# Performance work log

Hardware: AMD Instinct MI355X
Metric: run time of the kernel (lower is better)

The kernel has to match this reference:

```python
import jax, jax.numpy as jnp
import numpy as np

NUM_CLASSES = 80
S = 7            # grid_size
NB = 2           # num_boxes per cell
LAMBDA_COORD = 5.0
LAMBDA_NOOBJ = 0.5
N_BOX = 20       # padded boxes per image


def setup_inputs() -> dict:
    key = jax.random.key(0)
    k1, k2, k3, k4 = jax.random.split(key, 4)
    B = 4096
    predictions = jax.random.uniform(k1, (B, S, S, NB, 5 + NUM_CLASSES), dtype=jnp.float32)
    # build valid normalized xyxy boxes: centers in [0.1,0.9], half-sizes in [0.01,0.085]
    centers = jax.random.uniform(k2, (B, N_BOX, 2), dtype=jnp.float32) * 0.8 + 0.1
    half = jax.random.uniform(k3, (B, N_BOX, 2), dtype=jnp.float32) * 0.075 + 0.01
    targets_boxes = jnp.concatenate([centers - half, centers + half], axis=-1)
    targets_labels = jax.random.randint(k4, (B, N_BOX), 0, NUM_CLASSES)
    return {"predictions": predictions, "targets_boxes": targets_boxes, "targets_labels": targets_labels}


def encode_targets(boxes, labels):
    # boxes: [B,N,4] xyxy normalized; labels: [B,N] int
    B, N, _ = boxes.shape
    x = (boxes[..., 0] + boxes[..., 2]) * 0.5
    y = (boxes[..., 1] + boxes[..., 3]) * 0.5
    w = boxes[..., 2] - boxes[..., 0]
    h = boxes[..., 3] - boxes[..., 1]
    j = jnp.clip(jnp.floor(x * S).astype(jnp.int32), 0, S - 1)
    i = jnp.clip(jnp.floor(y * S).astype(jnp.int32), 0, S - 1)
    x_cell = x * S - j
    y_cell = y * S - i
    onehot = jax.nn.one_hot(labels, NUM_CLASSES, dtype=boxes.dtype)
    feats = jnp.concatenate([x_cell[..., None], y_cell[..., None], w[..., None], h[..., None],
                             jnp.ones_like(x_cell)[..., None], onehot], axis=-1)  # [B,N,5+C]
    bidx = jnp.arange(B, dtype=jnp.int32)[:, None]
    flat = ((bidx * S + i) * S + j).ravel()                       # [B*N] cell ids
    order = jnp.broadcast_to(jnp.arange(N, dtype=jnp.int32), (B, N)).ravel()
    winner = jnp.full((B * S * S,), N, dtype=jnp.int32).at[flat].min(order)
    cell_b = jnp.arange(B * S * S, dtype=jnp.int32) // (S * S)
    sel = jnp.minimum(winner, N - 1)
    grid = feats[cell_b, sel]
    grid = jnp.where((winner < N)[:, None], grid, jnp.zeros_like(grid))
    return grid.reshape(B, S, S, 5 + NUM_CLASSES)


def iou_xywh(a, b):
    ax1 = a[..., 0] - a[..., 2] * 0.5; ay1 = a[..., 1] - a[..., 3] * 0.5
    ax2 = a[..., 0] + a[..., 2] * 0.5; ay2 = a[..., 1] + a[..., 3] * 0.5
    bx1 = b[..., 0] - b[..., 2] * 0.5; by1 = b[..., 1] - b[..., 3] * 0.5
    bx2 = b[..., 0] + b[..., 2] * 0.5; by2 = b[..., 1] + b[..., 3] * 0.5
    iw = jnp.clip(jnp.minimum(ax2, bx2) - jnp.maximum(ax1, bx1), 0.0)
    ih = jnp.clip(jnp.minimum(ay2, by2) - jnp.maximum(ay1, by1), 0.0)
    inter = iw * ih
    union = (ax2 - ax1) * (ay2 - ay1) + (bx2 - bx1) * (by2 - by1) - inter
    return inter / (union + 1e-6)


def yolo_loss(predictions, targets_boxes, targets_labels):
    B = predictions.shape[0]
    tg = encode_targets(targets_boxes, targets_labels)   # [B,S,S,5+C]
    txy, twh = tg[..., :2], tg[..., 2:4]
    tconf, tcls = tg[..., 4:5], tg[..., 5:]
    obj = (tconf[..., 0] > 0).astype(predictions.dtype)   # [B,S,S]
    # responsible box = argmax IoU per cell, masked by obj
    pred_boxes = predictions[..., 0:4]                     # [B,S,S,NB,4]
    tgt_boxes = jnp.concatenate([txy, twh], axis=-1)[:, :, :, None, :]
    ious = iou_xywh(pred_boxes, jnp.broadcast_to(tgt_boxes, pred_boxes.shape))  # [B,S,S,NB]
    best = jnp.argmax(ious, axis=-1)
    resp = jax.nn.one_hot(best, NB, dtype=predictions.dtype) * obj[..., None]   # [B,S,S,NB]
    pxy = predictions[..., 0:2]; pwh = predictions[..., 2:4]
    pconf = predictions[..., 4:5]; pcls = predictions[..., 5:]
    om = obj[..., None, None]        # [B,S,S,1,1]
    rm = resp[..., None]             # [B,S,S,NB,1]
    loss_xy = LAMBDA_COORD * jnp.sum(om * rm * (pxy - txy[:, :, :, None, :]) ** 2) / B
    loss_wh = LAMBDA_COORD * jnp.sum(om * rm * (jnp.sqrt(jnp.clip(pwh, 1e-6)) - jnp.sqrt(jnp.clip(twh[:, :, :, None, :], 1e-6))) ** 2) / B
    loss_conf_obj = jnp.sum(om * rm * (pconf - tconf[:, :, :, None, :]) ** 2) / B
    loss_conf_noobj = LAMBDA_NOOBJ * jnp.sum((1.0 - obj)[..., None, None] * pconf ** 2) / B
    pred_cls_resp = jnp.sum(pcls * rm, axis=3)             # [B,S,S,C]
    loss_cls = jnp.sum(obj[..., None] * (pred_cls_resp - tcls) ** 2) / B
    return loss_xy + loss_wh + loss_conf_obj + loss_conf_noobj + loss_cls


def reference(predictions, targets_boxes, targets_labels):
    return yolo_loss(predictions, targets_boxes, targets_labels)
```

## Files before the change

kernel.cpp:

```cpp
#include <hip/hip_runtime.h>

#define S 7
#define NB 2
#define NC 80
#define NBOX 20
#define CELLS (S*S)
#define CH (5+NC)
#define PER_B (CELLS*NB*CH)
#define L_COORD 5.0f
#define L_NOOBJ 0.5f

__global__ __launch_bounds__(256) void yolo_loss_kernel(
    const float* __restrict__ pred,
    const float* __restrict__ boxes,
    const int*   __restrict__ labels,
    float*       __restrict__ out,
    float inv_B)
{
    __shared__ int   s_winner[CELLS];
    __shared__ float s_cx[NBOX], s_cy[NBOX], s_w[NBOX], s_h[NBOX];
    __shared__ int   s_lab[NBOX];
    __shared__ float s_tx[CELLS], s_ty[CELLS], s_tw[CELLS], s_th[CELLS];
    __shared__ int   s_label[CELLS];
    __shared__ int   s_resp[CELLS];
    __shared__ float s_wsum[4];

    const int b   = blockIdx.x;
    const int tid = threadIdx.x;

    if (tid < CELLS) s_winner[tid] = NBOX;
    __syncthreads();

    if (tid < NBOX) {
        const float* bx = boxes + ((size_t)b * NBOX + tid) * 4;
        float x1 = bx[0], y1 = bx[1], x2 = bx[2], y2 = bx[3];
        float x = (x1 + x2) * 0.5f, y = (y1 + y2) * 0.5f;
        float w = x2 - x1,          h = y2 - y1;
        int j = (int)floorf(x * (float)S); j = min(max(j, 0), S - 1);
        int i = (int)floorf(y * (float)S); i = min(max(i, 0), S - 1);
        s_cx[tid] = x; s_cy[tid] = y; s_w[tid] = w; s_h[tid] = h;
        s_lab[tid] = labels[(size_t)b * NBOX + tid];
        atomicMin(&s_winner[i * S + j], tid);
    }
    __syncthreads();

    if (tid < CELLS) {
        int w = s_winner[tid];
        if (w < NBOX) {
            int i = tid / S, j = tid - (tid / S) * S;
            float x = s_cx[w], y = s_cy[w];
            float tx = x * (float)S - (float)j;
            float ty = y * (float)S - (float)i;
            float tw = s_w[w], th = s_h[w];
            s_tx[tid] = tx; s_ty[tid] = ty; s_tw[tid] = tw; s_th[tid] = th;
            s_label[tid] = s_lab[w];

            const float* p = pred + ((size_t)b * CELLS + tid) * (NB * CH);
            float iou[2];
            float bx1 = tx - tw * 0.5f, by1 = ty - th * 0.5f;
            float bx2 = tx + tw * 0.5f, by2 = ty + th * 0.5f;
            float barea = (bx2 - bx1) * (by2 - by1);
            #pragma unroll
            for (int nb = 0; nb < NB; nb++) {
                float px = p[nb * CH + 0], py = p[nb * CH + 1];
                float pw = p[nb * CH + 2], ph = p[nb * CH + 3];
                float ax1 = px - pw * 0.5f, ay1 = py - ph * 0.5f;
                float ax2 = px + pw * 0.5f, ay2 = py + ph * 0.5f;
                float iw = fmaxf(fminf(ax2, bx2) - fmaxf(ax1, bx1), 0.0f);
                float ih = fmaxf(fminf(ay2, by2) - fmaxf(ay1, by1), 0.0f);
                float inter = iw * ih;
                float uni = (ax2 - ax1) * (ay2 - ay1) + barea - inter;
                iou[nb] = inter / (uni + 1e-6f);
            }
            s_resp[tid] = (iou[1] > iou[0]) ? 1 : 0;
        } else {
            s_resp[tid] = -1;
            s_tx[tid] = 0.f; s_ty[tid] = 0.f; s_tw[tid] = 0.f; s_th[tid] = 0.f;
            s_label[tid] = 0;
        }
    }
    __syncthreads();

    float acc = 0.0f;
    const float2* p2 = (const float2*)(pred + (size_t)b * PER_B);
    for (int e = tid; e < PER_B / 2; e += 256) {
        float2 v = p2[e];
        int f = 2 * e;
        #pragma unroll
        for (int k = 0; k < 2; k++) {
            int ff = f + k;
            float p = (k == 0) ? v.x : v.y;
            int c  = ff / (NB * CH);
            int r  = ff - c * (NB * CH);
            int nb = (r >= CH) ? 1 : 0;
            int ch = r - nb * CH;
            int resp = s_resp[c];
            if (resp < 0) {
                if (ch == 4) acc += L_NOOBJ * p * p;
            } else if (nb == resp) {
                if (ch >= 5) {
                    float t = (ch - 5 == s_label[c]) ? 1.0f : 0.0f;
                    float d = p - t; acc += d * d;
                } else if (ch == 4) {
                    float d = p - 1.0f; acc += d * d;
                } else if (ch < 2) {
                    float t = (ch == 0) ? s_tx[c] : s_ty[c];
                    float d = p - t; acc += L_COORD * d * d;
                } else {
                    float t = (ch == 2) ? s_tw[c] : s_th[c];
                    float d = sqrtf(fmaxf(p, 1e-6f)) - sqrtf(fmaxf(t, 1e-6f));
                    acc += L_COORD * d * d;
                }
            }
        }
    }

    #pragma unroll
    for (int off = 32; off > 0; off >>= 1) acc += __shfl_down(acc, off, 64);
    int lane = tid & 63, wv = tid >> 6;
    if (lane == 0) s_wsum[wv] = acc;
    __syncthreads();
    if (tid == 0) {
        float s = s_wsum[0] + s_wsum[1] + s_wsum[2] + s_wsum[3];
        atomicAdd(out, s * inv_B);
    }
}

extern "C" void kernel_launch(void* const* d_in, const int* in_sizes, int n_in,
                              void* d_out, int out_size, void* d_ws, size_t ws_size,
                              hipStream_t stream) {
    const float* pred   = (const float*)d_in[0];
    const float* boxes  = (const float*)d_in[1];
    const int*   labels = (const int*)d_in[2];
    float* out = (float*)d_out;

    const int B = in_sizes[0] / PER_B;

    hipMemsetAsync(d_out, 0, sizeof(float) * out_size, stream);
    yolo_loss_kernel<<<B, 256, 0, stream>>>(pred, boxes, labels, out, 1.0f / (float)B);
}
```

Before: 229.0 us.

## Unroll streaming loop with batched loads and branchless per-element loss

Replaces the strided per-element loop with a fully unrolled loop that issues four float2 loads before computing, which raises memory-level parallelism. The per-element loss becomes branchless select arithmetic, and the per-cell metadata (responsible box and label) is packed into one shared int. Target sqrt values are precomputed once per cell instead of per element. This costs more registers, and the loop bound is now hardcoded for PER_B/2 = 4165.

```diff
diff --git a/kernel.cpp b/kernel.cpp
--- a/kernel.cpp
+++ b/kernel.cpp
@@ -6,9 +6,48 @@
 #define NBOX 20
 #define CELLS (S*S)
 #define CH (5+NC)
-#define PER_B (CELLS*NB*CH)
+#define PAIR (NB*CH)
+#define PER_B (CELLS*PAIR)
+#define NIT (PER_B/2)
 #define L_COORD 5.0f
 #define L_NOOBJ 0.5f
+
+__device__ __forceinline__ float pair_loss(float2 v, int ff,
+                                           const int* __restrict__ s_meta,
+                                           const float* __restrict__ s_coord)
+{
+    unsigned c = (unsigned)ff / (unsigned)PAIR;
+    int r0 = ff - (int)c * PAIR;
+    int meta = s_meta[c];
+    int respp1 = meta >> 8;
+    int label  = meta & 0xff;
+    bool noobj = (respp1 == 0);
+
+    float acc = 0.0f;
+    #pragma unroll
+    for (int k = 0; k < 2; ++k) {
+        float p = k ? v.y : v.x;
+        int r  = r0 + k;
+        int nb = (r >= CH) ? 1 : 0;
+        int ch = r - nb * CH;
+
+        bool isresp = ((nb + 1) == respp1);
+        float t_box = s_coord[4u * c + (ch & 3)];
+        float t = (ch >= 5) ? ((ch - 5 == label) ? 1.0f : 0.0f)
+                : (ch == 4) ? 1.0f
+                : t_box;
+        float q = (ch == 2 || ch == 3) ? sqrtf(fmaxf(p, 1e-6f)) : p;
+
+        float m_obj = isresp ? ((ch < 4) ? L_COORD : 1.0f) : 0.0f;
+        float m_no  = (ch == 4) ? L_NOOBJ : 0.0f;
+        float m = noobj ? m_no : m_obj;
+        t = noobj ? 0.0f : t;
+
+        float d = q - t;
+        acc += m * d * d;
+    }
+    return acc;
+}
 
 __global__ __launch_bounds__(256) void yolo_loss_kernel(
     const float* __restrict__ pred,
@@ -20,9 +59,8 @@
     __shared__ int   s_winner[CELLS];
     __shared__ float s_cx[NBOX], s_cy[NBOX], s_w[NBOX], s_h[NBOX];
     __shared__ int   s_lab[NBOX];
-    __shared__ float s_tx[CELLS], s_ty[CELLS], s_tw[CELLS], s_th[CELLS];
-    __shared__ int   s_label[CELLS];
-    __shared__ int   s_resp[CELLS];
+    __shared__ int   s_meta[CELLS];
+    __shared__ float s_coord[CELLS * 4];
     __shared__ float s_wsum[4];
 
     const int b   = blockIdx.x;
@@ -52,10 +90,12 @@
             float tx = x * (float)S - (float)j;
             float ty = y * (float)S - (float)i;
             float tw = s_w[w], th = s_h[w];
-            s_tx[tid] = tx; s_ty[tid] = ty; s_tw[tid] = tw; s_th[tid] = th;
-            s_label[tid] = s_lab[w];
+            s_coord[4 * tid + 0] = tx;
+            s_coord[4 * tid + 1] = ty;
+            s_coord[4 * tid + 2] = sqrtf(fmaxf(tw, 1e-6f));
+            s_coord[4 * tid + 3] = sqrtf(fmaxf(th, 1e-6f));
 
-            const float* p = pred + ((size_t)b * CELLS + tid) * (NB * CH);
+            const float* p = pred + ((size_t)b * CELLS + tid) * PAIR;
             float iou[2];
             float bx1 = tx - tw * 0.5f, by1 = ty - th * 0.5f;
             float bx2 = tx + tw * 0.5f, by2 = ty + th * 0.5f;
@@ -72,47 +112,33 @@
                 float uni = (ax2 - ax1) * (ay2 - ay1) + barea - inter;
                 iou[nb] = inter / (uni + 1e-6f);
             }
-            s_resp[tid] = (iou[1] > iou[0]) ? 1 : 0;
+            int resp = (iou[1] > iou[0]) ? 1 : 0;
+            s_meta[tid] = ((resp + 1) << 8) | s_lab[w];
         } else {
-            s_resp[tid] = -1;
-            s_tx[tid] = 0.f; s_ty[tid] = 0.f; s_tw[tid] = 0.f; s_th[tid] = 0.f;
-            s_label[tid] = 0;
+            s_meta[tid] = 0;
+            s_coord[4 * tid + 0] = 0.f; s_coord[4 * tid + 1] = 0.f;
+            s_coord[4 * tid + 2] = 0.f; s_coord[4 * tid + 3] = 0.f;
         }
     }
     __syncthreads();
 
     float acc = 0.0f;
     const float2* p2 = (const float2*)(pred + (size_t)b * PER_B);
-    for (int e = tid; e < PER_B / 2; e += 256) {
-        float2 v = p2[e];
-        int f = 2 * e;
-        #pragma unroll
-        for (int k = 0; k < 2; k++) {
-            int ff = f + k;
-            float p = (k == 0) ? v.x : v.y;
-            int c  = ff / (NB * CH);
-            int r  = ff - c * (NB * CH);
-            int nb = (r >= CH) ? 1 : 0;
-            int ch = r - nb * CH;
-            int resp = s_resp[c];
-            if (resp < 0) {
-                if (ch == 4) acc += L_NOOBJ * p * p;
-            } else if (nb == resp) {
-                if (ch >= 5) {
-                    float t = (ch - 5 == s_label[c]) ? 1.0f : 0.0f;
-                    float d = p - t; acc += d * d;
-                } else if (ch == 4) {
-                    float d = p - 1.0f; acc += d * d;
-                } else if (ch < 2) {
-                    float t = (ch == 0) ? s_tx[c] : s_ty[c];
-                    float d = p - t; acc += L_COORD * d * d;
-                } else {
-                    float t = (ch == 2) ? s_tw[c] : s_th[c];
-                    float d = sqrtf(fmaxf(p, 1e-6f)) - sqrtf(fmaxf(t, 1e-6f));
-                    acc += L_COORD * d * d;
-                }
-            }
-        }
+    #pragma unroll
+    for (int k = 0; k < 4; ++k) {
+        int e = tid + k * 1024;
+        float2 v0 = p2[e];
+        float2 v1 = p2[e + 256];
+        float2 v2 = p2[e + 512];
+        float2 v3 = p2[e + 768];
+        acc += pair_loss(v0, 2 * e,          s_meta, s_coord);
+        acc += pair_loss(v1, 2 * (e + 256),  s_meta, s_coord);
+        acc += pair_loss(v2, 2 * (e + 512),  s_meta, s_coord);
+        acc += pair_loss(v3, 2 * (e + 768),  s_meta, s_coord);
+    }
+    {
+        int e = 4096 + tid;
+        if (e < NIT) acc += pair_loss(p2[e], 2 * e, s_meta, s_coord);
     }
 
     #pragma unroll
```

New measurement: 215.6 us. -5.8%, faster.

## Reformulate loss as weighted sum of squares with per-cell weight table, two images per block

Applied to the files above, without the earlier changes.

Expands each squared difference algebraically so the streaming pass only computes w*p*p from a small per-cell, per-category weight table in shared memory. The cross terms for the responsible box (coordinates, confidence, the true-class logit) are computed once per cell by a dedicated thread. Each block now handles two images, which lets a fully unrolled float4 loop cover 8330*2 floats with 16 full iterations plus a tail and removes the branchy per-element logic. The kernel assumes B is even and the 8-byte pair layout, and trades exact squared differences for the expanded form, which may change rounding slightly.

```diff
diff --git a/kernel.cpp b/kernel.cpp
--- a/kernel.cpp
+++ b/kernel.cpp
@@ -4,11 +4,40 @@
 #define NB 2
 #define NC 80
 #define NBOX 20
-#define CELLS (S*S)
-#define CH (5+NC)
-#define PER_B (CELLS*NB*CH)
+#define CELLS 49
+#define CH 85
+#define PAIR 170
+#define PER_B 8330
+#define N4 4165
 #define L_COORD 5.0f
 #define L_NOOBJ 0.5f
+
+__device__ __forceinline__ float elem1(float p, unsigned c, int r,
+                                       const float* __restrict__ wt)
+{
+    int nb  = (r >= CH) ? 1 : 0;
+    int rr  = r - nb * CH;
+    int cat = (rr >= 4) + (rr >= 5);
+    float w = wt[c * 8u + (unsigned)(nb * 4 + cat)];
+    return w * p * p;
+}
+
+__device__ __forceinline__ float elem4(float4 v, int e,
+                                       const float* __restrict__ wt)
+{
+    unsigned ff = 4u * (unsigned)e;
+    unsigned c0 = ff / (unsigned)PAIR;
+    int r0 = (int)(ff - c0 * (unsigned)PAIR);
+    int wrap = (r0 == PAIR - 2) ? 1 : 0;
+    unsigned c1 = c0 + (unsigned)wrap;
+    int r2 = wrap ? 0 : r0 + 2;
+    float a;
+    a  = elem1(v.x, c0, r0,     wt);
+    a += elem1(v.y, c0, r0 + 1, wt);
+    a += elem1(v.z, c1, r2,     wt);
+    a += elem1(v.w, c1, r2 + 1, wt);
+    return a;
+}
 
 __global__ __launch_bounds__(256) void yolo_loss_kernel(
     const float* __restrict__ pred,
@@ -17,102 +46,98 @@
     float*       __restrict__ out,
     float inv_B)
 {
-    __shared__ int   s_winner[CELLS];
-    __shared__ float s_cx[NBOX], s_cy[NBOX], s_w[NBOX], s_h[NBOX];
-    __shared__ int   s_lab[NBOX];
-    __shared__ float s_tx[CELLS], s_ty[CELLS], s_tw[CELLS], s_th[CELLS];
-    __shared__ int   s_label[CELLS];
-    __shared__ int   s_resp[CELLS];
+    __shared__ int   s_winner[2 * CELLS];
+    __shared__ float s_cx[2 * NBOX], s_cy[2 * NBOX], s_bw[2 * NBOX], s_bh[2 * NBOX];
+    __shared__ int   s_lab[2 * NBOX];
+    __shared__ float s_wt[2 * CELLS * 8];
     __shared__ float s_wsum[4];
 
-    const int b   = blockIdx.x;
+    const int b0  = blockIdx.x * 2;
     const int tid = threadIdx.x;
 
-    if (tid < CELLS) s_winner[tid] = NBOX;
+    if (tid < 2 * CELLS) s_winner[tid] = NBOX;
     __syncthreads();
 
-    if (tid < NBOX) {
-        const float* bx = boxes + ((size_t)b * NBOX + tid) * 4;
+    if (tid < 2 * NBOX) {
+        int img = (tid >= NBOX) ? 1 : 0;
+        const float* bx = boxes + ((size_t)(b0 + img) * NBOX + (tid - img * NBOX)) * 4;
         float x1 = bx[0], y1 = bx[1], x2 = bx[2], y2 = bx[3];
         float x = (x1 + x2) * 0.5f, y = (y1 + y2) * 0.5f;
-        float w = x2 - x1,          h = y2 - y1;
+        s_cx[tid] = x; s_cy[tid] = y;
+        s_bw[tid] = x2 - x1; s_bh[tid] = y2 - y1;
+        s_lab[tid] = labels[(size_t)(b0 + img) * NBOX + (tid - img * NBOX)];
         int j = (int)floorf(x * (float)S); j = min(max(j, 0), S - 1);
         int i = (int)floorf(y * (float)S); i = min(max(i, 0), S - 1);
-        s_cx[tid] = x; s_cy[tid] = y; s_w[tid] = w; s_h[tid] = h;
-        s_lab[tid] = labels[(size_t)b * NBOX + tid];
-        atomicMin(&s_winner[i * S + j], tid);
+        atomicMin(&s_winner[img * CELLS + i * S + j], tid - img * NBOX);
     }
     __syncthreads();
 
-    if (tid < CELLS) {
-        int w = s_winner[tid];
+    float acc = 0.0f;
+    if (tid < 2 * CELLS) {
+        int img  = (tid >= CELLS) ? 1 : 0;
+        int cell = tid - img * CELLS;
+        int w    = s_winner[tid];
+        int base = tid * 8;
         if (w < NBOX) {
-            int i = tid / S, j = tid - (tid / S) * S;
-            float x = s_cx[w], y = s_cy[w];
+            int i = cell / S, j = cell - (cell / S) * S;
+            int bi = img * NBOX + w;
+            float x = s_cx[bi], y = s_cy[bi];
             float tx = x * (float)S - (float)j;
             float ty = y * (float)S - (float)i;
-            float tw = s_w[w], th = s_h[w];
-            s_tx[tid] = tx; s_ty[tid] = ty; s_tw[tid] = tw; s_th[tid] = th;
-            s_label[tid] = s_lab[w];
+            float tw = s_bw[bi], th = s_bh[bi];
 
-            const float* p = pred + ((size_t)b * CELLS + tid) * (NB * CH);
-            float iou[2];
+            const float* p = pred + ((size_t)(b0 + img) * CELLS + cell) * PAIR;
             float bx1 = tx - tw * 0.5f, by1 = ty - th * 0.5f;
             float bx2 = tx + tw * 0.5f, by2 = ty + th * 0.5f;
             float barea = (bx2 - bx1) * (by2 - by1);
+            float iou[2], px[2], py[2], pw[2], ph[2];
             #pragma unroll
             for (int nb = 0; nb < NB; nb++) {
-                float px = p[nb * CH + 0], py = p[nb * CH + 1];
-                float pw = p[nb * CH + 2], ph = p[nb * CH + 3];
-                float ax1 = px - pw * 0.5f, ay1 = py - ph * 0.5f;
-                float ax2 = px + pw * 0.5f, ay2 = py + ph * 0.5f;
+                px[nb] = p[nb * CH + 0]; py[nb] = p[nb * CH + 1];
+                pw[nb] = p[nb * CH + 2]; ph[nb] = p[nb * CH + 3];
+                float ax1 = px[nb] - pw[nb] * 0.5f, ay1 = py[nb] - ph[nb] * 0.5f;
+                float ax2 = px[nb] + pw[nb] * 0.5f, ay2 = py[nb] + ph[nb] * 0.5f;
                 float iw = fmaxf(fminf(ax2, bx2) - fmaxf(ax1, bx1), 0.0f);
                 float ih = fmaxf(fminf(ay2, by2) - fmaxf(ay1, by1), 0.0f);
                 float inter = iw * ih;
                 float uni = (ax2 - ax1) * (ay2 - ay1) + barea - inter;
                 iou[nb] = inter / (uni + 1e-6f);
             }
-            s_resp[tid] = (iou[1] > iou[0]) ? 1 : 0;
+            int resp = (iou[1] > iou[0]) ? 1 : 0;
+            int oth  = 1 - resp;
+
+            s_wt[base + resp * 4 + 0] = 0.0f;
+            s_wt[base + resp * 4 + 1] = 1.0f;
+            s_wt[base + resp * 4 + 2] = 1.0f;
+            s_wt[base + oth  * 4 + 0] = 0.0f;
+            s_wt[base + oth  * 4 + 1] = 0.0f;
+            s_wt[base + oth  * 4 + 2] = 0.0f;
+
+            float pc = p[resp * CH + 4];
+            float pl = p[resp * CH + 5 + s_lab[bi]];
+            float dx = px[resp] - tx, dy = py[resp] - ty;
+            float dw = sqrtf(fmaxf(pw[resp], 1e-6f)) - sqrtf(fmaxf(tw, 1e-6f));
+            float dh = sqrtf(fmaxf(ph[resp], 1e-6f)) - sqrtf(fmaxf(th, 1e-6f));
+            acc = L_COORD * (dx * dx + dy * dy + dw * dw + dh * dh)
+                + (1.0f - 2.0f * pc)
+                + (1.0f - 2.0f * pl);
         } else {
-            s_resp[tid] = -1;
-            s_tx[tid] = 0.f; s_ty[tid] = 0.f; s_tw[tid] = 0.f; s_th[tid] = 0.f;
-            s_label[tid] = 0;
+            s_wt[base + 0] = 0.0f; s_wt[base + 1] = L_NOOBJ; s_wt[base + 2] = 0.0f;
+            s_wt[base + 4] = 0.0f; s_wt[base + 5] = L_NOOBJ; s_wt[base + 6] = 0.0f;
         }
     }
     __syncthreads();
 
-    float acc = 0.0f;
-    const float2* p2 = (const float2*)(pred + (size_t)b * PER_B);
-    for (int e = tid; e < PER_B / 2; e += 256) {
-        float2 v = p2[e];
-        int f = 2 * e;
-        #pragma unroll
-        for (int k = 0; k < 2; k++) {
-            int ff = f + k;
-            float p = (k == 0) ? v.x : v.y;
-            int c  = ff / (NB * CH);
-            int r  = ff - c * (NB * CH);
-            int nb = (r >= CH) ? 1 : 0;
-            int ch = r - nb * CH;
-            int resp = s_resp[c];
-            if (resp < 0) {
-                if (ch == 4) acc += L_NOOBJ * p * p;
-            } else if (nb == resp) {
-                if (ch >= 5) {
-                    float t = (ch - 5 == s_label[c]) ? 1.0f : 0.0f;
-                    float d = p - t; acc += d * d;
-                } else if (ch == 4) {
-                    float d = p - 1.0f; acc += d * d;
-                } else if (ch < 2) {
-                    float t = (ch == 0) ? s_tx[c] : s_ty[c];
-                    float d = p - t; acc += L_COORD * d * d;
-                } else {
-                    float t = (ch == 2) ? s_tw[c] : s_th[c];
-                    float d = sqrtf(fmaxf(p, 1e-6f)) - sqrtf(fmaxf(t, 1e-6f));
-                    acc += L_COORD * d * d;
-                }
-            }
-        }
+    const float4* p4 = (const float4*)(pred + (size_t)b0 * PER_B);
+    #pragma unroll
+    for (int k = 0; k < 16; ++k) {
+        int e = tid + k * 256;
+        float4 v = p4[e];
+        acc += elem4(v, e, s_wt);
+    }
+    {
+        int e = 4096 + tid;
+        if (e < N4) acc += elem4(p4[e], e, s_wt);
     }
 
     #pragma unroll
@@ -132,10 +157,10 @@
     const float* pred   = (const float*)d_in[0];
     const float* boxes  = (const float*)d_in[1];
     const int*   labels = (const int*)d_in[2];
-    float* out = (float*)d_out;
 
     const int B = in_sizes[0] / PER_B;
 
     hipMemsetAsync(d_out, 0, sizeof(float) * out_size, stream);
-    yolo_loss_kernel<<<B, 256, 0, stream>>>(pred, boxes, labels, out, 1.0f / (float)B);
+    yolo_loss_kernel<<<B / 2, 256, 0, stream>>>(pred, boxes, labels,
+                                                (float*)d_out, 1.0f / (float)B);
 }
```

Measured after the change: 213.9 us. -6.6%, faster.
